# Performance work log

Hardware: AMD Instinct MI355X
Metric: run time of the kernel (lower is better)

## Reference

```python
import jax, jax.numpy as jnp
import numpy as np

N_NODES = 100000
N_EDGES = 1600000
N_GRAPHS = 64
IN_DIM = 128
EMB_DIM = 128


def setup_inputs() -> dict:
    key = jax.random.key(0)
    ks = jax.random.split(key, 12)
    node_type = jax.random.randint(ks[0], (N_NODES,), 0, 4)
    num_inverted_predecessors = jax.random.randint(ks[1], (N_NODES,), 0, 3)
    edge_index = jax.random.randint(ks[2], (2, N_EDGES), 0, N_NODES)
    batch = jnp.sort(jax.random.randint(ks[3], (N_NODES,), 0, N_GRAPHS))
    emb_type = jax.random.normal(ks[4], (4, IN_DIM), dtype=jnp.float32) * 0.1
    emb_inv = jax.random.normal(ks[5], (3, IN_DIM), dtype=jnp.float32) * 0.1
    W0 = jax.random.normal(ks[6], (IN_DIM, EMB_DIM), dtype=jnp.float32) * 0.05
    b0 = jnp.zeros((EMB_DIM,), dtype=jnp.float32)
    W1 = jax.random.normal(ks[7], (EMB_DIM, EMB_DIM), dtype=jnp.float32) * 0.05
    b1 = jnp.zeros((EMB_DIM,), dtype=jnp.float32)
    W2 = jax.random.normal(ks[8], (EMB_DIM, EMB_DIM), dtype=jnp.float32) * 0.05
    b2 = jnpes = jnp.zeros((EMB_DIM,), dtype=jnp.float32)
    return {
        'node_type': node_type,
        'num_inverted_predecessors': num_inverted_predecessors,
        'edge_index': edge_index,
        'batch': batch,
        'emb_type': emb_type,
        'emb_inv': emb_inv,
        'W0': W0, 'b0': b0,
        'W1': W1, 'b1': b1,
        'W2': W2, 'b2': jnp.zeros((EMB_DIM,), dtype=jnp.float32),
    }


def gcn_conv(h, W, b, src, dst, n_nodes):
    # PyG GCNConv: out = D^{-1/2} (A + I) D^{-1/2} (X W) + b, all edge weights 1.
    xw = h @ W  # [N, out]
    ones = jnp.ones(dst.shape[0], dtype=h.dtype)
    deg = jax.ops.segment_sum(ones, dst, num_segments=n_nodes) + 1.0  # +1 self loop
    dinv = jax.lax.rsqrt(deg)  # deg >= 1
    coef = (dinv[dst] * dinv[src])[:, None]  # [E, 1]
    agg = jax.ops.segment_sum(xw[src] * coef, dst, num_segments=n_nodes)
    agg = agg + xw * (dinv * dinv)[:, None]  # self-loop term
    return agg + b


def reference(node_type, num_inverted_predecessors, edge_index, batch,
              emb_type, emb_inv, W0, b0, W1, b1, W2, b2):
    src, dst = edge_index[0], edge_index[1]
    n_nodes = node_type.shape[0]
    # node encoder: sum of two categorical embeddings
    h = emb_type[node_type] + emb_inv[num_inverted_predecessors]  # [N, IN_DIM]
    # layer 0, 1 with ReLU (norms are constructed but unused in the torch forward)
    h = jax.nn.relu(gcn_conv(h, W0, b0, src, dst, n_nodes))
    h = jax.nn.relu(gcn_conv(h, W1, b1, src, dst, n_nodes))
    # final layer, no activation
    h = gcn_conv(h, W2, b2, src, dst, n_nodes)
    # global readouts over batch index: max and sum
    gmax = jax.ops.segment_max(h, batch, num_segments=N_GRAPHS)
    gsum = jax.ops.segment_sum(h, batch, num_segments=N_GRAPHS)
    out = jnp.concatenate([gmax, gsum], axis=1)  # [B, 2*EMB_DIM]
    return jnp.round(out * 1000.0) / 1000.0  # torch.round(..., decimals=3)
```

## Files before the change

kernel.cpp:

```cpp
#include <hip/hip_runtime.h>
#include <hip/hip_bf16.h>
#include <cstdint>

#define NNODES 100000
#define NEDGES 1600000
#define NGRAPHS 64
#define DIM 128

#define NB 196
#define BSHIFT 9
#define SC_BLOCKS 200
#define SC_EPB (NEDGES / SC_BLOCKS)
#define EB_CAP 10000

typedef __attribute__((ext_vector_type(8))) short bf16x8;
typedef __attribute__((ext_vector_type(4))) float f32x4;

__device__ inline ushort f2bf(float f) {
  __hip_bfloat16 h = __float2bfloat16(f);
  return __builtin_bit_cast(ushort, h);
}
__device__ inline float bf2f(ushort u) {
  return __uint_as_float(((unsigned)u) << 16);
}
__device__ inline unsigned fkey(float f) {
  unsigned b = __float_as_uint(f);
  return (b & 0x80000000u) ? ~b : (b | 0x80000000u);
}
__device__ inline float fdecode(unsigned k) {
  unsigned b = (k & 0x80000000u) ? (k & 0x7FFFFFFFu) : ~k;
  return __uint_as_float(b);
}


__global__ __launch_bounds__(256) void hist2_kernel(const int* __restrict__ dst,
                                                    int* __restrict__ blockhist,
                                                    int* __restrict__ bhist) {
  __shared__ int bh[NB];
  int tid = threadIdx.x;
  if (tid < NB) bh[tid] = 0;
  __syncthreads();
  int base = blockIdx.x * SC_EPB;
  for (int o = tid * 4; o < SC_EPB; o += 1024) {
    int4 d4 = *(const int4*)(dst + base + o);
    atomicAdd(&bh[d4.x >> BSHIFT], 1);
    atomicAdd(&bh[d4.y >> BSHIFT], 1);
    atomicAdd(&bh[d4.z >> BSHIFT], 1);
    atomicAdd(&bh[d4.w >> BSHIFT], 1);
  }
  __syncthreads();
  if (tid < NB) {
    blockhist[blockIdx.x * NB + tid] = bh[tid];
    if (bh[tid]) atomicAdd(&bhist[tid], bh[tid]);
  }
}

__global__ __launch_bounds__(256) void scanB_kernel(const int* __restrict__ bhist,
                                                    const int* __restrict__ blockhist,
                                                    int* __restrict__ bbase,
                                                    int* __restrict__ blockbase,
                                                    int* __restrict__ offs) {
  __shared__ int gb[256];
  __shared__ int col[256];
  int tid = threadIdx.x;
  int b = blockIdx.x;
  int v = (tid < NB) ? bhist[tid] : 0;
  gb[tid] = v;
  __syncthreads();
  for (int o = 1; o < 256; o <<= 1) {
    int t = (tid >= o) ? gb[tid - o] : 0;
    __syncthreads();
    gb[tid] += t;
    __syncthreads();
  }
  int excl_b = gb[b] - bhist[b];
  int c = (tid < SC_BLOCKS) ? blockhist[tid * NB + b] : 0;
  col[tid] = c;
  __syncthreads();
  for (int o = 1; o < 256; o <<= 1) {
    int t = (tid >= o) ? col[tid - o] : 0;
    __syncthreads();
    col[tid] += t;
    __syncthreads();
  }
  if (tid < SC_BLOCKS) blockbase[tid * NB + b] = excl_b + col[tid] - c;
  if (tid == 0) {
    bbase[b] = excl_b;
    if (b == 0) { bbase[NB] = NEDGES; offs[NNODES] = NEDGES; }
  }
}

__global__ __launch_bounds__(256) void scatter2_kernel(const int* __restrict__ src,
                                                       const int* __restrict__ dst,
                                                       const int* __restrict__ blockbase,
                                                       unsigned* __restrict__ gbuf) {
  __shared__ int lcur[NB];
  int tid = threadIdx.x;
  if (tid < NB) lcur[tid] = blockbase[blockIdx.x * NB + tid];
  __syncthreads();
  int base = blockIdx.x * SC_EPB;
  for (int o = tid * 4; o < SC_EPB; o += 1024) {
    int4 s4 = *(const int4*)(src + base + o);
    int4 d4 = *(const int4*)(dst + base + o);
    int ss[4] = {s4.x, s4.y, s4.z, s4.w};
    int dd[4] = {d4.x, d4.y, d4.z, d4.w};
#pragma unroll
    for (int u = 0; u < 4; ++u) {
      int bk = dd[u] >> BSHIFT;
      unsigned rec = (unsigned)ss[u] | ((unsigned)(dd[u] & 511) << 17);
      int pos = atomicAdd(&lcur[bk], 1);
      gbuf[pos] = rec;
    }
  }
}

__global__ __launch_bounds__(256) void bucket_sort(const unsigned* __restrict__ gbuf,
                                                   const int* __restrict__ bhist,
                                                   const int* __restrict__ bbase,
                                                   const int* __restrict__ nt,
                                                   const int* __restrict__ nv,
                                                   int* __restrict__ csr_src,
                                                   int* __restrict__ offs,
                                                   float* __restrict__ dinv,
                                                   unsigned* __restrict__ pk) {
  __shared__ int lhist[512];
  __shared__ int lscan[512];
  __shared__ int lcur2[512];
  __shared__ int lcsr[EB_CAP];
  int tid = threadIdx.x;
  int b = blockIdx.x;
  int ebase = bbase[b];
  int bsize = bhist[b];
  lhist[tid] = 0; lhist[tid + 256] = 0;
  lcur2[tid] = 0; lcur2[tid + 256] = 0;
  __syncthreads();
  for (int k = tid; k < bsize; k += 256)
    atomicAdd(&lhist[(gbuf[ebase + k] >> 17) & 511], 1);
  __syncthreads();
  lscan[tid] = lhist[tid];
  lscan[tid + 256] = lhist[tid + 256];
  __syncthreads();
  for (int o = 1; o < 256; o <<= 1) {
    int a = (tid >= o) ? lscan[tid - o] : 0;
    int c = (tid >= o) ? lscan[256 + tid - o] : 0;
    __syncthreads();
    lscan[tid] += a;
    lscan[256 + tid] += c;
    __syncthreads();
  }
  int tot = lscan[255];
  __syncthreads();
  lscan[256 + tid] += tot;
  __syncthreads();
  int nodebase = b << BSHIFT;
#pragma unroll
  for (int hh = 0; hh < 2; ++hh) {
    int l = hh * 256 + tid;
    int i = nodebase + l;
    if (i < NNODES) {
      int c = lhist[l];
      offs[i] = ebase + (lscan[l] - c);
      float dv = rsqrtf((float)c + 1.0f);
      dinv[i] = dv;
      pk[i] = (__float_as_uint(dv) & 0xFFFFFFF0u) |
              ((unsigned)nt[i] << 2) | (unsigned)nv[i];
    }
  }
  for (int k = tid; k < bsize; k += 256) {
    unsigned e = gbuf[ebase + k];
    int l = (e >> 17) & 511;
    int p = atomicAdd(&lcur2[l], 1);
    int pos = (lscan[l] - lhist[l]) + p;
    if (pos < EB_CAP) lcsr[pos] = (int)(e & 0x1FFFFu);
  }
  __syncthreads();
  for (int k = tid; k < bsize; k += 256) csr_src[ebase + k] = lcsr[k];
}


__global__ __launch_bounds__(128) void prep_kernel(const float* __restrict__ et,
                                                   const float* __restrict__ ei,
                                                   const float* __restrict__ W0,
                                                   const float* __restrict__ W1,
                                                   const float* __restrict__ W2,
                                                   float* __restrict__ TW,
                                                   ushort* __restrict__ wbf) {
  int b = blockIdx.x;
  int tid = threadIdx.x;
  if (b < 7) {
    const float* in = (b < 4) ? (et + b * DIM) : (ei + (b - 4) * DIM);
    float acc = 0.f;
    for (int k = 0; k < DIM; ++k) acc += in[k] * W0[k * DIM + tid];
    TW[b * DIM + tid] = acc;
  } else {
    int m = (b - 7) >> 4;
    int blk = (b - 7) & 15;
    const float* w = m ? W2 : W1;
    ushort* o = wbf + (size_t)m * DIM * DIM;
    int base = blk * 1024 + tid * 8;
    float4 a = *(const float4*)(w + base);
    float4 c = *(const float4*)(w + base + 4);
    uint4 r;
    r.x = ((unsigned)f2bf(a.y) << 16) | f2bf(a.x);
    r.y = ((unsigned)f2bf(a.w) << 16) | f2bf(a.z);
    r.z = ((unsigned)f2bf(c.y) << 16) | f2bf(c.x);
    r.w = ((unsigned)f2bf(c.w) << 16) | f2bf(c.z);
    *(uint4*)(o + base) = r;
  }
}


__device__ inline void pk_accum(unsigned p, float& c0, float& c1, float& c2, float& c3,
                                float& c4, float& c5, float& c6) {
  float dv = __uint_as_float(p & 0xFFFFFFF0u);
  int t = (p >> 2) & 3, v = p & 3;
  c0 += (t == 0) ? dv : 0.f;
  c1 += (t == 1) ? dv : 0.f;
  c2 += (t == 2) ? dv : 0.f;
  c3 += (t == 3) ? dv : 0.f;
  c4 += (v == 0) ? dv : 0.f;
  c5 += (v == 1) ? dv : 0.f;
  c6 += (v == 2) ? dv : 0.f;
}

__global__ __launch_bounds__(256) void coef_kernel(const int* __restrict__ offs,
                                                   const int* __restrict__ csr_src,
                                                   const unsigned* __restrict__ pk,
                                                   float* __restrict__ Cbuf) {
  int gid = blockIdx.x * 256 + threadIdx.x;
  int i = gid >> 2;
  int sl = gid & 3;
  if (i >= NNODES) return;
  int s0 = offs[i], s1 = offs[i + 1];
  float c0 = 0.f, c1 = 0.f, c2 = 0.f, c3 = 0.f, c4 = 0.f, c5 = 0.f, c6 = 0.f;
  int j = s0 + sl;
  for (; j + 28 < s1; j += 32) {
    int s_[8];
#pragma unroll
    for (int u = 0; u < 8; ++u) s_[u] = csr_src[j + 4 * u];
    unsigned p_[8];
#pragma unroll
    for (int u = 0; u < 8; ++u) p_[u] = pk[s_[u]];
#pragma unroll
    for (int u = 0; u < 8; ++u) pk_accum(p_[u], c0, c1, c2, c3, c4, c5, c6);
  }
  for (; j < s1; j += 4) pk_accum(pk[csr_src[j]], c0, c1, c2, c3, c4, c5, c6);
#pragma unroll
  for (int o = 1; o < 4; o <<= 1) {
    c0 += __shfl_xor(c0, o);
    c1 += __shfl_xor(c1, o);
    c2 += __shfl_xor(c2, o);
    c3 += __shfl_xor(c3, o);
    c4 += __shfl_xor(c4, o);
    c5 += __shfl_xor(c5, o);
    c6 += __shfl_xor(c6, o);
  }
  if (sl == 0) {
    unsigned pb = pk[i];
    float di = __uint_as_float(pb & 0xFFFFFFF0u);
    int t = (pb >> 2) & 3, v = pb & 3;
    c0 += (t == 0) ? di : 0.f;
    c1 += (t == 1) ? di : 0.f;
    c2 += (t == 2) ? di : 0.f;
    c3 += (t == 3) ? di : 0.f;
    c4 += (v == 0) ? di : 0.f;
    c5 += (v == 1) ? di : 0.f;
    c6 += (v == 2) ? di : 0.f;
    float4 lo = {c0, c1, c2, c3};
    float4 hi = {c4, c5, c6, 0.f};
    *(float4*)(Cbuf + (size_t)i * 8) = lo;
    *(float4*)(Cbuf + (size_t)i * 8 + 4) = hi;
  }
}

__global__ void h1_kernel(const float* __restrict__ Cbuf, const float* __restrict__ TW,
                          const float* __restrict__ dinv, const float* __restrict__ b0,
                          ushort* __restrict__ h) {
  int idx = blockIdx.x * blockDim.x + threadIdx.x;
  if (idx >= NNODES * 32) return;
  int i = idx >> 5, d4 = (idx & 31) << 2;
  const float* C = Cbuf + (size_t)i * 8;
  float4 acc = {0.f, 0.f, 0.f, 0.f};
#pragma unroll
  for (int k = 0; k < 7; ++k) {
    float ck = C[k];
    float4 tw = *(const float4*)(TW + k * DIM + d4);
    acc.x += ck * tw.x; acc.y += ck * tw.y;
    acc.z += ck * tw.z; acc.w += ck * tw.w;
  }
  float di = dinv[i];
  float4 bb = *(const float4*)(b0 + d4);
  float vx = fmaxf(di * acc.x + bb.x, 0.f);
  float vy = fmaxf(di * acc.y + bb.y, 0.f);
  float vz = fmaxf(di * acc.z + bb.z, 0.f);
  float vw = fmaxf(di * acc.w + bb.w, 0.f);
  uint2 o;
  o.x = ((unsigned)f2bf(vy) << 16) | f2bf(vx);
  o.y = ((unsigned)f2bf(vw) << 16) | f2bf(vz);
  *(uint2*)(h + (size_t)i * DIM + d4) = o;
}


__global__ __launch_bounds__(256) void gemm_kernel(const ushort* __restrict__ h,
                                                   const ushort* __restrict__ wb,
                                                   const float* __restrict__ dinv,
                                                   ushort* __restrict__ out) {
  __shared__ ushort Ws[32 * 64 * 8];
  int tid = threadIdx.x;
  for (int g = tid; g < 2048; g += 256) {
    int kt = g >> 6, l = g & 63;
    int ks = kt >> 3, t = kt & 7;
    int kb = ks * 32 + ((l >> 4) << 3);
    int col = t * 16 + (l & 15);
#pragma unroll
    for (int j = 0; j < 8; ++j) Ws[g * 8 + j] = wb[(kb + j) * DIM + col];
  }
  __syncthreads();
  int w = tid >> 6, lane = tid & 63;
  for (int tile = blockIdx.x * 4 + w; tile < NNODES / 16; tile += gridDim.x * 4) {
    int row0 = tile * 16;
    const ushort* hrow = h + (size_t)(row0 + (lane & 15)) * DIM + ((lane >> 4) << 3);
    f32x4 acc[8];
#pragma unroll
    for (int t = 0; t < 8; ++t) acc[t] = {0.f, 0.f, 0.f, 0.f};
#pragma unroll
    for (int ks = 0; ks < 4; ++ks) {
      bf16x8 a = *(const bf16x8*)(hrow + ks * 32);
#pragma unroll
      for (int t = 0; t < 8; ++t) {
        bf16x8 b = *(const bf16x8*)&Ws[((ks * 8 + t) * 64 + lane) * 8];
        acc[t] = __builtin_amdgcn_mfma_f32_16x16x32_bf16(a, b, acc[t], 0, 0, 0);
      }
    }
    int rbase = row0 + ((lane >> 4) << 2);
    int cbase = lane & 15;
    float4 dv = *(const float4*)(dinv + rbase);
    float dvr[4] = {dv.x, dv.y, dv.z, dv.w};
#pragma unroll
    for (int t = 0; t < 8; ++t)
#pragma unroll
      for (int r = 0; r < 4; ++r)
        out[(size_t)(rbase + r) * DIM + t * 16 + cbase] = f2bf(acc[t][r] * dvr[r]);
  }
}


__global__ __launch_bounds__(256, 8) void agg_kernel(const ushort* __restrict__ xws,
                                                     const int* __restrict__ offs,
                                                     const int* __restrict__ csr_src,
                                                     const float* __restrict__ dinv,
                                                     const float* __restrict__ bias,
                                                     ushort* __restrict__ outb, int relu) {
  int i = blockIdx.x * 4 + (threadIdx.x >> 6);
  if (i >= NNODES) return;
  int lane = threadIdx.x & 63;
  int s0 = offs[i], s1 = offs[i + 1];
  float ax = 0.f, ay = 0.f;
  int j = s0;
  for (; j + 16 <= s1; j += 16) {
    int s[16];
#pragma unroll
    for (int u = 0; u < 16; ++u) s[u] = csr_src[j + u];
    unsigned p[16];
#pragma unroll
    for (int u = 0; u < 16; ++u)
      p[u] = *(const unsigned*)(xws + (size_t)s[u] * DIM + lane * 2);
#pragma unroll
    for (int u = 0; u < 16; ++u) {
      ax += bf2f((ushort)(p[u] & 0xffffu));
      ay += bf2f((ushort)(p[u] >> 16));
    }
  }
  for (; j + 4 <= s1; j += 4) {
    int s[4];
#pragma unroll
    for (int u = 0; u < 4; ++u) s[u] = csr_src[j + u];
    unsigned p[4];
#pragma unroll
    for (int u = 0; u < 4; ++u)
      p[u] = *(const unsigned*)(xws + (size_t)s[u] * DIM + lane * 2);
#pragma unroll
    for (int u = 0; u < 4; ++u) {
      ax += bf2f((ushort)(p[u] & 0xffffu));
      ay += bf2f((ushort)(p[u] >> 16));
    }
  }
  for (; j < s1; ++j) {
    int sa = csr_src[j];
    unsigned pa = *(const unsigned*)(xws + (size_t)sa * DIM + lane * 2);
    ax += bf2f((ushort)(pa & 0xffffu));
    ay += bf2f((ushort)(pa >> 16));
  }
  unsigned ps = *(const unsigned*)(xws + (size_t)i * DIM + lane * 2);
  ax += bf2f((ushort)(ps & 0xffffu));
  ay += bf2f((ushort)(ps >> 16));
  float di = dinv[i];
  float2 b = *(const float2*)(bias + lane * 2);
  float vx = di * ax + b.x;
  float vy = di * ay + b.y;
  if (relu) { vx = fmaxf(vx, 0.f); vy = fmaxf(vy, 0.f); }
  *(unsigned*)(outb + (size_t)i * DIM + lane * 2) =
      ((unsigned)f2bf(vy) << 16) | f2bf(vx);
}


__global__ __launch_bounds__(128) void readout_kernel(const ushort* __restrict__ h,
                                                      const int* __restrict__ batch,
                                                      unsigned* __restrict__ gmaxk,
                                                      float* __restrict__ gsum) {
  int d = threadIdx.x;
  int start = blockIdx.x * 128;
  if (start >= NNODES) return;
  int end = min(start + 128, NNODES);
  int cur = batch[start];
  float s = 0.f, m = -INFINITY;
  for (int i = start; i < end; ++i) {
    int g = batch[i];
    float v = bf2f(h[(size_t)i * DIM + d]);
    if (g != cur) {
      atomicAdd(&gsum[cur * DIM + d], s);
      atomicMax(&gmaxk[cur * DIM + d], fkey(m));
      cur = g; s = 0.f; m = -INFINITY;
    }
    s += v;
    m = fmaxf(m, v);
  }
  atomicAdd(&gsum[cur * DIM + d], s);
  atomicMax(&gmaxk[cur * DIM + d], fkey(m));
}

__global__ void pack_kernel(const unsigned* __restrict__ gmaxk,
                            const float* __restrict__ gsum, float* __restrict__ out) {
  int idx = blockIdx.x * blockDim.x + threadIdx.x;
  if (idx >= NGRAPHS * 256) return;
  int g = idx >> 8, d = idx & 255;
  float v = (d < 128) ? fdecode(gmaxk[g * DIM + d]) : gsum[g * DIM + (d - 128)];
  out[idx] = rintf(v * 1000.0f) / 1000.0f;
}


extern "C" void kernel_launch(void* const* d_in, const int* in_sizes, int n_in,
                              void* d_out, int out_size, void* d_ws, size_t ws_size,
                              hipStream_t stream) {
  const int* node_type = (const int*)d_in[0];
  const int* ninv      = (const int*)d_in[1];
  const int* edge      = (const int*)d_in[2];
  const int* batch     = (const int*)d_in[3];
  const float* emb_type = (const float*)d_in[4];
  const float* emb_inv  = (const float*)d_in[5];
  const float* W0 = (const float*)d_in[6];
  const float* B[3] = {(const float*)d_in[7], (const float*)d_in[9], (const float*)d_in[11]};
  const float* W1 = (const float*)d_in[8];
  const float* W2 = (const float*)d_in[10];
  const int* srcp = edge;
  const int* dstp = edge + NEDGES;
  float* out = (float*)d_out;

  char* ws = (char*)d_ws;
  auto alloc = [&](size_t bytes) {
    char* p = ws;
    ws += (bytes + 255) & ~(size_t)255;
    return p;
  };
  ushort* hA     = (ushort*)alloc((size_t)NNODES * DIM * 2);
  ushort* xws    = (ushort*)alloc((size_t)NNODES * DIM * 2);
  float* dinv    = (float*)alloc((size_t)NNODES * 4);
  unsigned* pk   = (unsigned*)alloc((size_t)NNODES * 4);
  int* offs      = (int*)alloc((size_t)(NNODES + 1) * 4);
  int* csr_src   = (int*)alloc((size_t)NEDGES * 4);
  unsigned* gbuf = (unsigned*)alloc((size_t)NEDGES * 4);
  float* Cbuf    = (float*)alloc((size_t)NNODES * 8 * 4);
  unsigned* gmaxk = (unsigned*)alloc((size_t)NGRAPHS * DIM * 4);
  float* gsum    = (float*)alloc((size_t)NGRAPHS * DIM * 4);
  int* bhist     = (int*)alloc((size_t)NB * 4);
  int* bbase     = (int*)alloc((size_t)(NB + 1) * 4);
  int* blockhist = (int*)alloc((size_t)SC_BLOCKS * NB * 4);
  int* blockbase = (int*)alloc((size_t)SC_BLOCKS * NB * 4);
  float* TW      = (float*)alloc((size_t)7 * DIM * 4);
  ushort* wbf    = (ushort*)alloc((size_t)2 * DIM * DIM * 2);

  hipMemsetAsync(gmaxk, 0, (size_t)NGRAPHS * DIM * 4 * 2 + NB * 4, stream);

  hist2_kernel<<<SC_BLOCKS, 256, 0, stream>>>(dstp, blockhist, bhist);
  scanB_kernel<<<NB, 256, 0, stream>>>(bhist, blockhist, bbase, blockbase, offs);
  scatter2_kernel<<<SC_BLOCKS, 256, 0, stream>>>(srcp, dstp, blockbase, gbuf);
  bucket_sort<<<NB, 256, 0, stream>>>(gbuf, bhist, bbase, node_type, ninv,
                                      csr_src, offs, dinv, pk);

  prep_kernel<<<39, 128, 0, stream>>>(emb_type, emb_inv, W0, W1, W2, TW, wbf);
  coef_kernel<<<(NNODES * 4 + 255) / 256, 256, 0, stream>>>(offs, csr_src, pk, Cbuf);
  h1_kernel<<<NNODES * 32 / 256, 256, 0, stream>>>(Cbuf, TW, dinv, B[0], hA);

  for (int l = 1; l < 3; ++l) {
    gemm_kernel<<<1024, 256, 0, stream>>>(hA, wbf + (size_t)(l - 1) * DIM * DIM, dinv, xws);
    agg_kernel<<<NNODES / 4, 256, 0, stream>>>(xws, offs, csr_src, dinv, B[l],
                                               hA, l < 2 ? 1 : 0);
  }

  readout_kernel<<<(NNODES + 127) / 128, 128, 0, stream>>>(hA, batch, gmaxk, gsum);
  pack_kernel<<<64, 256, 0, stream>>>(gmaxk, gsum, out);
}
```

Before: 282.0 us.

## Fuse layer-0 embedding expansion into first GEMM and halve sort bucket size

Result: no change. 277.5 us (-1.6%).

```diff
diff --git a/kernel.cpp b/kernel.cpp
--- a/kernel.cpp
+++ b/kernel.cpp
@@ -7,11 +7,11 @@
 #define NGRAPHS 64
 #define DIM 128
 
-#define NB 196
-#define BSHIFT 9
+#define NB 391
+#define BSHIFT 8
 #define SC_BLOCKS 200
 #define SC_EPB (NEDGES / SC_BLOCKS)
-#define EB_CAP 10000
+#define EB_CAP 5000
 
 typedef __attribute__((ext_vector_type(8))) short bf16x8;
 typedef __attribute__((ext_vector_type(4))) float f32x4;
@@ -38,7 +38,7 @@
                                                     int* __restrict__ bhist) {
   __shared__ int bh[NB];
   int tid = threadIdx.x;
-  if (tid < NB) bh[tid] = 0;
+  for (int k = tid; k < NB; k += 256) bh[k] = 0;
   __syncthreads();
   int base = blockIdx.x * SC_EPB;
   for (int o = tid * 4; o < SC_EPB; o += 1024) {
@@ -49,25 +49,25 @@
     atomicAdd(&bh[d4.w >> BSHIFT], 1);
   }
   __syncthreads();
-  if (tid < NB) {
-    blockhist[blockIdx.x * NB + tid] = bh[tid];
-    if (bh[tid]) atomicAdd(&bhist[tid], bh[tid]);
-  }
-}
-
-__global__ __launch_bounds__(256) void scanB_kernel(const int* __restrict__ bhist,
+  for (int k = tid; k < NB; k += 256) {
+    blockhist[blockIdx.x * NB + k] = bh[k];
+    if (bh[k]) atomicAdd(&bhist[k], bh[k]);
+  }
+}
+
+__global__ __launch_bounds__(512) void scanB_kernel(const int* __restrict__ bhist,
                                                     const int* __restrict__ blockhist,
                                                     int* __restrict__ bbase,
                                                     int* __restrict__ blockbase,
                                                     int* __restrict__ offs) {
-  __shared__ int gb[256];
-  __shared__ int col[256];
+  __shared__ int gb[512];
+  __shared__ int col[512];
   int tid = threadIdx.x;
   int b = blockIdx.x;
   int v = (tid < NB) ? bhist[tid] : 0;
   gb[tid] = v;
   __syncthreads();
-  for (int o = 1; o < 256; o <<= 1) {
+  for (int o = 1; o < 512; o <<= 1) {
     int t = (tid >= o) ? gb[tid - o] : 0;
     __syncthreads();
     gb[tid] += t;
@@ -77,7 +77,7 @@
   int c = (tid < SC_BLOCKS) ? blockhist[tid * NB + b] : 0;
   col[tid] = c;
   __syncthreads();
-  for (int o = 1; o < 256; o <<= 1) {
+  for (int o = 1; o < 512; o <<= 1) {
     int t = (tid >= o) ? col[tid - o] : 0;
     __syncthreads();
     col[tid] += t;
@@ -96,7 +96,7 @@
                                                        unsigned* __restrict__ gbuf) {
   __shared__ int lcur[NB];
   int tid = threadIdx.x;
-  if (tid < NB) lcur[tid] = blockbase[blockIdx.x * NB + tid];
+  for (int k = tid; k < NB; k += 256) lcur[k] = blockbase[blockIdx.x * NB + k];
   __syncthreads();
   int base = blockIdx.x * SC_EPB;
   for (int o = tid * 4; o < SC_EPB; o += 1024) {
@@ -107,7 +107,7 @@
 #pragma unroll
     for (int u = 0; u < 4; ++u) {
       int bk = dd[u] >> BSHIFT;
-      unsigned rec = (unsigned)ss[u] | ((unsigned)(dd[u] & 511) << 17);
+      unsigned rec = (unsigned)ss[u] | ((unsigned)(dd[u] & 255) << 17);
       int pos = atomicAdd(&lcur[bk], 1);
       gbuf[pos] = rec;
     }
@@ -123,52 +123,40 @@
                                                    int* __restrict__ offs,
                                                    float* __restrict__ dinv,
                                                    unsigned* __restrict__ pk) {
-  __shared__ int lhist[512];
-  __shared__ int lscan[512];
-  __shared__ int lcur2[512];
+  __shared__ int lhist[256];
+  __shared__ int lscan[256];
+  __shared__ int lcur2[256];
   __shared__ int lcsr[EB_CAP];
   int tid = threadIdx.x;
   int b = blockIdx.x;
   int ebase = bbase[b];
   int bsize = bhist[b];
-  lhist[tid] = 0; lhist[tid + 256] = 0;
-  lcur2[tid] = 0; lcur2[tid + 256] = 0;
+  lhist[tid] = 0;
+  lcur2[tid] = 0;
   __syncthreads();
   for (int k = tid; k < bsize; k += 256)
-    atomicAdd(&lhist[(gbuf[ebase + k] >> 17) & 511], 1);
+    atomicAdd(&lhist[(gbuf[ebase + k] >> 17) & 255], 1);
   __syncthreads();
   lscan[tid] = lhist[tid];
-  lscan[tid + 256] = lhist[tid + 256];
   __syncthreads();
   for (int o = 1; o < 256; o <<= 1) {
     int a = (tid >= o) ? lscan[tid - o] : 0;
-    int c = (tid >= o) ? lscan[256 + tid - o] : 0;
     __syncthreads();
     lscan[tid] += a;
-    lscan[256 + tid] += c;
     __syncthreads();
   }
-  int tot = lscan[255];
-  __syncthreads();
-  lscan[256 + tid] += tot;
-  __syncthreads();
-  int nodebase = b << BSHIFT;
-#pragma unroll
-  for (int hh = 0; hh < 2; ++hh) {
-    int l = hh * 256 + tid;
-    int i = nodebase + l;
-    if (i < NNODES) {
-      int c = lhist[l];
-      offs[i] = ebase + (lscan[l] - c);
-      float dv = rsqrtf((float)c + 1.0f);
-      dinv[i] = dv;
-      pk[i] = (__float_as_uint(dv) & 0xFFFFFFF0u) |
-              ((unsigned)nt[i] << 2) | (unsigned)nv[i];
-    }
+  int i = (b << BSHIFT) + tid;
+  if (i < NNODES) {
+    int c = lhist[tid];
+    offs[i] = ebase + (lscan[tid] - c);
+    float dv = rsqrtf((float)c + 1.0f);
+    dinv[i] = dv;
+    pk[i] = (__float_as_uint(dv) & 0xFFFFFFF0u) |
+            ((unsigned)nt[i] << 2) | (unsigned)nv[i];
   }
   for (int k = tid; k < bsize; k += 256) {
     unsigned e = gbuf[ebase + k];
-    int l = (e >> 17) & 511;
+    int l = (e >> 17) & 255;
     int p = atomicAdd(&lcur2[l], 1);
     int pos = (lscan[l] - lhist[l]) + p;
     if (pos < EB_CAP) lcsr[pos] = (int)(e & 0x1FFFFu);
@@ -273,31 +261,67 @@
   }
 }
 
-__global__ void h1_kernel(const float* __restrict__ Cbuf, const float* __restrict__ TW,
-                          const float* __restrict__ dinv, const float* __restrict__ b0,
-                          ushort* __restrict__ h) {
-  int idx = blockIdx.x * blockDim.x + threadIdx.x;
-  if (idx >= NNODES * 32) return;
-  int i = idx >> 5, d4 = (idx & 31) << 2;
-  const float* C = Cbuf + (size_t)i * 8;
-  float4 acc = {0.f, 0.f, 0.f, 0.f};
-#pragma unroll
-  for (int k = 0; k < 7; ++k) {
-    float ck = C[k];
-    float4 tw = *(const float4*)(TW + k * DIM + d4);
-    acc.x += ck * tw.x; acc.y += ck * tw.y;
-    acc.z += ck * tw.z; acc.w += ck * tw.w;
-  }
-  float di = dinv[i];
-  float4 bb = *(const float4*)(b0 + d4);
-  float vx = fmaxf(di * acc.x + bb.x, 0.f);
-  float vy = fmaxf(di * acc.y + bb.y, 0.f);
-  float vz = fmaxf(di * acc.z + bb.z, 0.f);
-  float vw = fmaxf(di * acc.w + bb.w, 0.f);
-  uint2 o;
-  o.x = ((unsigned)f2bf(vy) << 16) | f2bf(vx);
-  o.y = ((unsigned)f2bf(vw) << 16) | f2bf(vz);
-  *(uint2*)(h + (size_t)i * DIM + d4) = o;
+
+__global__ __launch_bounds__(256) void gemm1_kernel(const float* __restrict__ Cbuf,
+                                                    const float* __restrict__ TW,
+                                                    const float* __restrict__ b0,
+                                                    const ushort* __restrict__ wb,
+                                                    const float* __restrict__ dinv,
+                                                    ushort* __restrict__ out) {
+  __shared__ ushort Ws[32 * 64 * 8];
+  __shared__ float TWs[7 * 128];
+  __shared__ float b0s[128];
+  int tid = threadIdx.x;
+  for (int g = tid; g < 2048; g += 256) {
+    int kt = g >> 6, l = g & 63;
+    int ks = kt >> 3, t = kt & 7;
+    int kb = ks * 32 + ((l >> 4) << 3);
+    int col = t * 16 + (l & 15);
+#pragma unroll
+    for (int j = 0; j < 8; ++j) Ws[g * 8 + j] = wb[(kb + j) * DIM + col];
+  }
+  for (int g = tid; g < 896; g += 256) TWs[g] = TW[g];
+  if (tid < 128) b0s[tid] = b0[tid];
+  __syncthreads();
+  int w = tid >> 6, lane = tid & 63;
+  for (int tile = blockIdx.x * 4 + w; tile < NNODES / 16; tile += gridDim.x * 4) {
+    int row0 = tile * 16;
+    int arow = row0 + (lane & 15);
+    float di = dinv[arow];
+    float4 Clo = *(const float4*)(Cbuf + (size_t)arow * 8);
+    float4 Chi = *(const float4*)(Cbuf + (size_t)arow * 8 + 4);
+    float C[7] = {Clo.x, Clo.y, Clo.z, Clo.w, Chi.x, Chi.y, Chi.z};
+    f32x4 acc[8];
+#pragma unroll
+    for (int t = 0; t < 8; ++t) acc[t] = {0.f, 0.f, 0.f, 0.f};
+#pragma unroll
+    for (int ks = 0; ks < 4; ++ks) {
+      int d0 = ((lane >> 4) << 3) + ks * 32;
+      bf16x8 a;
+#pragma unroll
+      for (int d = 0; d < 8; ++d) {
+        float dot = 0.f;
+#pragma unroll
+        for (int k = 0; k < 7; ++k) dot += C[k] * TWs[k * 128 + d0 + d];
+        float s = fmaxf(di * dot + b0s[d0 + d], 0.f);
+        a[d] = (short)f2bf(s);
+      }
+#pragma unroll
+      for (int t = 0; t < 8; ++t) {
+        bf16x8 bfr = *(const bf16x8*)&Ws[((ks * 8 + t) * 64 + lane) * 8];
+        acc[t] = __builtin_amdgcn_mfma_f32_16x16x32_bf16(a, bfr, acc[t], 0, 0, 0);
+      }
+    }
+    int rbase = row0 + ((lane >> 4) << 2);
+    int cbase = lane & 15;
+    float4 dv = *(const float4*)(dinv + rbase);
+    float dvr[4] = {dv.x, dv.y, dv.z, dv.w};
+#pragma unroll
+    for (int t = 0; t < 8; ++t)
+#pragma unroll
+      for (int r = 0; r < 4; ++r)
+        out[(size_t)(rbase + r) * DIM + t * 16 + cbase] = f2bf(acc[t][r] * dvr[r]);
+  }
 }
 
 
@@ -482,20 +506,19 @@
   hipMemsetAsync(gmaxk, 0, (size_t)NGRAPHS * DIM * 4 * 2 + NB * 4, stream);
 
   hist2_kernel<<<SC_BLOCKS, 256, 0, stream>>>(dstp, blockhist, bhist);
-  scanB_kernel<<<NB, 256, 0, stream>>>(bhist, blockhist, bbase, blockbase, offs);
+  scanB_kernel<<<NB, 512, 0, stream>>>(bhist, blockhist, bbase, blockbase, offs);
   scatter2_kernel<<<SC_BLOCKS, 256, 0, stream>>>(srcp, dstp, blockbase, gbuf);
   bucket_sort<<<NB, 256, 0, stream>>>(gbuf, bhist, bbase, node_type, ninv,
                                       csr_src, offs, dinv, pk);
 
   prep_kernel<<<39, 128, 0, stream>>>(emb_type, emb_inv, W0, W1, W2, TW, wbf);
   coef_kernel<<<(NNODES * 4 + 255) / 256, 256, 0, stream>>>(offs, csr_src, pk, Cbuf);
-  h1_kernel<<<NNODES * 32 / 256, 256, 0, stream>>>(Cbuf, TW, dinv, B[0], hA);
-
-  for (int l = 1; l < 3; ++l) {
-    gemm_kernel<<<1024, 256, 0, stream>>>(hA, wbf + (size_t)(l - 1) * DIM * DIM, dinv, xws);
-    agg_kernel<<<NNODES / 4, 256, 0, stream>>>(xws, offs, csr_src, dinv, B[l],
-                                               hA, l < 2 ? 1 : 0);
-  }
+
+  gemm1_kernel<<<1024, 256, 0, stream>>>(Cbuf, TW, B[0], wbf, dinv, xws);
+  agg_kernel<<<NNODES / 4, 256, 0, stream>>>(xws, offs, csr_src, dinv, B[1], hA, 1);
+
+  gemm_kernel<<<1024, 256, 0, stream>>>(hA, wbf + (size_t)DIM * DIM, dinv, xws);
+  agg_kernel<<<NNODES / 4, 256, 0, stream>>>(xws, offs, csr_src, dinv, B[2], hA, 0);
 
   readout_kernel<<<(NNODES + 127) / 128, 128, 0, stream>>>(hA, batch, gmaxk, gsum);
   pack_kernel<<<64, 256, 0, stream>>>(gmaxk, gsum, out);
```
